# Performance work log

Hardware: AMD Instinct MI355X
Metric: run time of the kernel (lower is better)

The kernel has to match this reference:

```python
import jax, jax.numpy as jnp
import numpy as np

IN_FEATURES = 4096
OUT_FEATURES = 4096
BLOCK_SIZE = 4096
NUM_BLOCKS = 4096
CODEBOOK_SIZE = 256
TOTAL_WEIGHTS = OUT_FEATURES * IN_FEATURES


def setup_inputs() -> dict:
    key = jax.random.key(0)
    k_x, k_cb, k_b, k_idx = jax.random.split(key, 4)
    x = jax.random.normal(k_x, (4, 2048, IN_FEATURES), dtype=jnp.float32)
    codebook = jax.random.normal(k_cb, (NUM_BLOCKS, CODEBOOK_SIZE), dtype=jnp.float32)
    bias = jax.random.normal(k_b, (OUT_FEATURES,), dtype=jnp.float32)
    indices = jax.random.randint(k_idx, (NUM_BLOCKS, BLOCK_SIZE), 0, CODEBOOK_SIZE, dtype=jnp.int64)
    return {"x": x, "codebook": codebook, "bias": bias, "indices": indices}


def reference(x, codebook, bias, indices):
    # weight = codebook[block_idx, indices] : per-block gather of codebook entries
    # codebook: [num_blocks, codebook_size], indices: [num_blocks, block_size]
    w_blocks = jnp.take_along_axis(codebook, indices, axis=1)  # [num_blocks, block_size]
    weight = w_blocks.reshape(-1)[:TOTAL_WEIGHTS].reshape(OUT_FEATURES, IN_FEATURES)
    # F.linear: x @ weight.T + bias
    return jnp.einsum("bsi,oi->bso", x, weight) + bias
```

## Files before the change

### kernel.cpp

```cpp
#include <hip/hip_runtime.h>

typedef __bf16 bf16x8 __attribute__((ext_vector_type(8)));
typedef float f32x4 __attribute__((ext_vector_type(4)));
typedef unsigned short u16x8 __attribute__((ext_vector_type(8)));
typedef int i32x4 __attribute__((ext_vector_type(4)));

#define M_TOT 8192
#define K_TOT 4096
#define N_TOT 4096
#define BM 256
#define BN 256
#define BK 64
#define NT (K_TOT / BK)

__device__ __forceinline__ unsigned short f2bf(float f) {
  union { float f; unsigned int u; } v; v.f = f;
  unsigned int u = v.u;
  return (unsigned short)((u + 0x7FFFu + ((u >> 16) & 1u)) >> 16);
}

__global__ __launch_bounds__(256) void deq_w(const float* __restrict__ cb,
                                             const int* __restrict__ idx,
                                             unsigned short* __restrict__ Wb) {
  size_t base = ((size_t)blockIdx.x * 256 + threadIdx.x) * 8;
  const float* crow = cb + ((base >> 12) << 8);
  i32x4 i0 = *(const i32x4*)(idx + base);
  i32x4 i1 = *(const i32x4*)(idx + base + 4);
  u16x8 o;
#pragma unroll
  for (int j = 0; j < 4; ++j) { o[j] = f2bf(crow[i0[j]]); o[4 + j] = f2bf(crow[i1[j]]); }
  *(u16x8*)(Wb + base) = o;
}

__global__ __launch_bounds__(256) void conv_x(const float* __restrict__ X,
                                              unsigned short* __restrict__ Xc) {
  size_t base = ((size_t)blockIdx.x * 256 + threadIdx.x) * 8;
  f32x4 a = *(const f32x4*)(X + base);
  f32x4 b = *(const f32x4*)(X + base + 4);
  u16x8 o;
#pragma unroll
  for (int j = 0; j < 4; ++j) { o[j] = f2bf(a[j]); o[4 + j] = f2bf(b[j]); }
  *(u16x8*)(Xc + base) = o;
}

#define GLDS16(g, l)                                                      \
  __builtin_amdgcn_global_load_lds(                                       \
      (__attribute__((address_space(1))) void*)(g),                       \
      (__attribute__((address_space(3))) void*)(l), 16, 0, 0)

__global__ __launch_bounds__(512, 2) void gemm8(const unsigned short* __restrict__ A,
                                                const unsigned short* __restrict__ B,
                                                const float* __restrict__ bias,
                                                float* __restrict__ C) {
  __shared__ __attribute__((aligned(128))) char lds[131072];

  const int tid = threadIdx.x;
  const int lane = tid & 63;
  const int wm = (tid >> 6) >> 2;
  const int wn = (tid >> 6) & 3;
  const int lr = lane & 15;

  const int bid = blockIdx.x;
  const int swz = (bid & 7) * 64 + (bid >> 3);
  const int bm = swz >> 4;
  const int bn = swz & 15;

  const unsigned short* Ap = A + (size_t)bm * BM * K_TOT;
  const unsigned short* Bp = B + (size_t)bn * BN * K_TOT;

  const int srow = tid >> 3;
  const int sgcol = (((tid & 7) * 16) ^ ((srow & 7) << 4)) >> 1;
  const int wavebase = (tid & 448) << 4;

  const int cs0 = (((lane >> 4) << 4)) ^ ((lr & 7) << 4);
  const int cs1 = (64 + ((lane >> 4) << 4)) ^ ((lr & 7) << 4);
  const int rowA0 = (wm * 128 + lr) * 128;
  const int rowB0 = 32768 + (wn * 64 + lr) * 128;

#define RD(off) (*(const bf16x8*)(lds + (off)))
#define STAGE(GB, TK, RB, LOFF)                                               \
  { _Pragma("unroll")                                                         \
    for (int ii = 0; ii < 2; ++ii) {                                          \
      GLDS16((GB) + (size_t)((RB) + ii * 64 + srow) * K_TOT + (TK) + sgcol,   \
             lds + (LOFF) + ii * 8192 + wavebase);                            \
    } }
#define BARRIER()                       \
  {                                     \
    asm volatile("" ::: "memory");      \
    __builtin_amdgcn_s_barrier();       \
    asm volatile("" ::: "memory");      \
  }

#define MFMA_Q(MH, AV, BV)                                                    \
  { __builtin_amdgcn_s_setprio(1);                                            \
    _Pragma("unroll")                                                         \
    for (int r = 0; r < 4; ++r) {                                             \
      _Pragma("unroll")                                                       \
      for (int nf = 0; nf < 4; ++nf)                                          \
        acc[(MH) * 4 + r][nf] = __builtin_amdgcn_mfma_f32_16x16x32_bf16(      \
            AV[r], BV[nf], acc[(MH) * 4 + r][nf], 0, 0, 0);                   \
    }                                                                         \
    __builtin_amdgcn_s_setprio(0); }

#define TILE(T, BO, STG_A, STG_B, VMF, DO_BAR)                                    \
  {                                                                               \
    bf16x8 Aa[4], Ab[4], Ac[4], Ad[4], Bx[4], By[4];                              \
    _Pragma("unroll") for (int r = 0; r < 4; ++r)                                 \
        Aa[r] = RD((BO) + rowA0 + r * 2048 + cs0);                                \
    _Pragma("unroll") for (int n = 0; n < 4; ++n)                                 \
        Bx[n] = RD((BO) + rowB0 + n * 2048 + cs0);                                \
    if (STG_A) STAGE(Ap, ((T) + 1) * BK, 0, ((BO) ^ 65536) + 0);                  \
    _Pragma("unroll") for (int r = 0; r < 4; ++r)                                 \
        Ab[r] = RD((BO) + rowA0 + (4 + r) * 2048 + cs0);                          \
    if (STG_A) STAGE(Ap, ((T) + 1) * BK, 128, ((BO) ^ 65536) + 16384);            \
    MFMA_Q(0, Aa, Bx);                                                            \
    _Pragma("unroll") for (int r = 0; r < 4; ++r)                                 \
        Ac[r] = RD((BO) + rowA0 + r * 2048 + cs1);                                \
    _Pragma("unroll") for (int n = 0; n < 4; ++n)                                 \
        By[n] = RD((BO) + rowB0 + n * 2048 + cs1);                                \
    MFMA_Q(1, Ab, Bx);                                                            \
    asm volatile("s_waitcnt lgkmcnt(0)" ::: "memory");                            \
    BARRIER();                                                                    \
    if (STG_B) STAGE(Bp, ((T) + 2) * BK, 0, (BO) + 32768);                        \
    if (STG_B) STAGE(Bp, ((T) + 2) * BK, 128, (BO) + 49152);                      \
    _Pragma("unroll") for (int r = 0; r < 4; ++r)                                 \
        Ad[r] = RD((BO) + rowA0 + (4 + r) * 2048 + cs1);                          \
    MFMA_Q(0, Ac, By);                                                            \
    MFMA_Q(1, Ad, By);                                                            \
    asm volatile("s_waitcnt vmcnt(" VMF ")" ::: "memory");                        \
    if (DO_BAR) BARRIER();                                                        \
  }

  f32x4 acc[8][4] = {};

  STAGE(Bp, 0, 0, 32768);
  STAGE(Bp, 0, 128, 49152);
  STAGE(Ap, 0, 0, 0);
  STAGE(Ap, 0, 128, 16384);
  STAGE(Bp, BK, 0, 65536 + 32768);
  STAGE(Bp, BK, 128, 65536 + 49152);
  asm volatile("s_waitcnt vmcnt(4)" ::: "memory");
  BARRIER();

  for (int t = 0; t < NT - 2; t += 2) {
    TILE(t,     0,     1, 1, "4", 1);
    TILE(t + 1, 65536, 1, 1, "4", 1);
  }
  TILE(NT - 2, 0,     1, 0, "0", 1);
  TILE(NT - 1, 65536, 0, 0, "0", 0);

  const int lg4 = (lane >> 4) << 2;
#pragma unroll
  for (int nf = 0; nf < 4; ++nf) {
    const int col = bn * BN + wn * 64 + nf * 16 + lr;
    const float bv = bias[col];
#pragma unroll
    for (int mf = 0; mf < 8; ++mf) {
      const int row0 = bm * BM + wm * 128 + mf * 16 + lg4;
      float* cp = C + (size_t)row0 * N_TOT + col;
#pragma unroll
      for (int j = 0; j < 4; ++j) cp[(size_t)j * N_TOT] = acc[mf][nf][j] + bv;
    }
  }
#undef RD
#undef STAGE
#undef BARRIER
#undef MFMA_Q
#undef TILE
}

extern "C" void kernel_launch(void* const* d_in, const int* in_sizes, int n_in,
                              void* d_out, int out_size, void* d_ws, size_t ws_size,
                              hipStream_t stream) {
  const float* x    = (const float*)d_in[0];
  const float* cb   = (const float*)d_in[1];
  const float* bias = (const float*)d_in[2];
  const int*   idx  = (const int*)d_in[3];

  float* out = (float*)d_out;

  unsigned short* Wb = (unsigned short*)d_ws;
  unsigned short* Xc = (unsigned short*)((char*)d_ws + (size_t)N_TOT * K_TOT * 2);

  deq_w<<<(N_TOT * (size_t)K_TOT) / (8 * 256), 256, 0, stream>>>(cb, idx, Wb);
  conv_x<<<((size_t)M_TOT * K_TOT) / (8 * 256), 256, 0, stream>>>(x, Xc);
  gemm8<<<512, 512, 0, stream>>>(Xc, Wb, bias, out);
}
```

Baseline: 274.1 us.

## Reorder GEMM tile into quadrant MFMA phases with scheduled LDS interleaving

Restructures each K-tile so every wave loads both K halves of its A and B fragments at once. It then issues MFMAs in four output quadrants, using sched_group_barrier to interleave the next quadrant's LDS reads with the current MFMAs. The B-stage global-to-LDS copies are split across the later quadrants, and the final tile now always ends with a barrier. The goal is to hide LDS read latency behind matrix work and smooth out the instruction mix. The cost is more explicit lgkmcnt waits, and the scheduling hints may not be honoured as intended.

```diff
diff --git a/kernel.cpp b/kernel.cpp
--- a/kernel.cpp
+++ b/kernel.cpp
@@ -90,45 +90,84 @@
     __builtin_amdgcn_s_barrier();       \
     asm volatile("" ::: "memory");      \
   }
-
-#define MFMA_Q(MH, AV, BV)                                                    \
-  { __builtin_amdgcn_s_setprio(1);                                            \
-    _Pragma("unroll")                                                         \
-    for (int r = 0; r < 4; ++r) {                                             \
-      _Pragma("unroll")                                                       \
-      for (int nf = 0; nf < 4; ++nf)                                          \
-        acc[(MH) * 4 + r][nf] = __builtin_amdgcn_mfma_f32_16x16x32_bf16(      \
-            AV[r], BV[nf], acc[(MH) * 4 + r][nf], 0, 0, 0);                   \
-    }                                                                         \
-    __builtin_amdgcn_s_setprio(0); }
-
-#define TILE(T, BO, STG_A, STG_B, VMF, DO_BAR)                                    \
+#define LGKM0() asm volatile("s_waitcnt lgkmcnt(0)" ::: "memory")
+#define SGB(mask, n) __builtin_amdgcn_sched_group_barrier((mask), (n), 0)
+
+#define QMF(MH, NH, AV, BV, MF)                                                          \
+  {                                                                                      \
+    acc[(MH)*4+(MF)][(NH)*2+0] = __builtin_amdgcn_mfma_f32_16x16x32_bf16(                \
+        AV[(MF)*2+0], BV[0], acc[(MH)*4+(MF)][(NH)*2+0], 0, 0, 0);                       \
+    acc[(MH)*4+(MF)][(NH)*2+0] = __builtin_amdgcn_mfma_f32_16x16x32_bf16(                \
+        AV[(MF)*2+1], BV[1], acc[(MH)*4+(MF)][(NH)*2+0], 0, 0, 0);                       \
+    acc[(MH)*4+(MF)][(NH)*2+1] = __builtin_amdgcn_mfma_f32_16x16x32_bf16(                \
+        AV[(MF)*2+0], BV[2], acc[(MH)*4+(MF)][(NH)*2+1], 0, 0, 0);                       \
+    acc[(MH)*4+(MF)][(NH)*2+1] = __builtin_amdgcn_mfma_f32_16x16x32_bf16(                \
+        AV[(MF)*2+1], BV[3], acc[(MH)*4+(MF)][(NH)*2+1], 0, 0, 0);                       \
+  }
+
+#define TILE(T, BO, STG_A, STG_B, VMF)                                            \
   {                                                                               \
-    bf16x8 Aa[4], Ab[4], Ac[4], Ad[4], Bx[4], By[4];                              \
-    _Pragma("unroll") for (int r = 0; r < 4; ++r)                                 \
-        Aa[r] = RD((BO) + rowA0 + r * 2048 + cs0);                                \
-    _Pragma("unroll") for (int n = 0; n < 4; ++n)                                 \
-        Bx[n] = RD((BO) + rowB0 + n * 2048 + cs0);                                \
+    bf16x8 Am[8], Am2[8], Bn[4], Bn2[4];                                          \
+     \
+    _Pragma("unroll") for (int r = 0; r < 4; ++r) {                               \
+      Am[r*2+0] = RD((BO) + rowA0 + r * 2048 + cs0);                              \
+      Am[r*2+1] = RD((BO) + rowA0 + r * 2048 + cs1);                              \
+    }                                                                             \
+    _Pragma("unroll") for (int n = 0; n < 2; ++n) {                               \
+      Bn[n*2+0] = RD((BO) + rowB0 + n * 2048 + cs0);                              \
+      Bn[n*2+1] = RD((BO) + rowB0 + n * 2048 + cs1);                              \
+    }                                                                             \
     if (STG_A) STAGE(Ap, ((T) + 1) * BK, 0, ((BO) ^ 65536) + 0);                  \
-    _Pragma("unroll") for (int r = 0; r < 4; ++r)                                 \
-        Ab[r] = RD((BO) + rowA0 + (4 + r) * 2048 + cs0);                          \
+    LGKM0();                                                                      \
+    __builtin_amdgcn_s_setprio(1);                                                \
+    QMF(0, 0, Am, Bn, 0);                                                         \
+    SGB(0x8, 4);                                                                  \
+    _Pragma("unroll") for (int n = 0; n < 2; ++n) {                               \
+      Bn2[n*2+0] = RD((BO) + rowB0 + 4096 + n * 2048 + cs0);                      \
+      Bn2[n*2+1] = RD((BO) + rowB0 + 4096 + n * 2048 + cs1);                      \
+    }                                                                             \
+    SGB(0x100, 4);                                                                \
+    QMF(0, 0, Am, Bn, 1);                                                         \
+    QMF(0, 0, Am, Bn, 2);                                                         \
+    QMF(0, 0, Am, Bn, 3);                                                         \
+    SGB(0x8, 12);                                                                 \
+    __builtin_amdgcn_s_setprio(0);                                                \
+     \
     if (STG_A) STAGE(Ap, ((T) + 1) * BK, 128, ((BO) ^ 65536) + 16384);            \
-    MFMA_Q(0, Aa, Bx);                                                            \
-    _Pragma("unroll") for (int r = 0; r < 4; ++r)                                 \
-        Ac[r] = RD((BO) + rowA0 + r * 2048 + cs1);                                \
-    _Pragma("unroll") for (int n = 0; n < 4; ++n)                                 \
-        By[n] = RD((BO) + rowB0 + n * 2048 + cs1);                                \
-    MFMA_Q(1, Ab, Bx);                                                            \
-    asm volatile("s_waitcnt lgkmcnt(0)" ::: "memory");                            \
+    LGKM0();                                                                      \
+    __builtin_amdgcn_s_setprio(1);                                                \
+    QMF(0, 1, Am, Bn2, 0);                                                        \
+    SGB(0x8, 4);                                                                  \
+    _Pragma("unroll") for (int r = 0; r < 4; ++r) {                               \
+      Am2[r*2+0] = RD((BO) + rowA0 + 8192 + r * 2048 + cs0);                      \
+      Am2[r*2+1] = RD((BO) + rowA0 + 8192 + r * 2048 + cs1);                      \
+    }                                                                             \
+    SGB(0x100, 8);                                                                \
+    QMF(0, 1, Am, Bn2, 1);                                                        \
+    QMF(0, 1, Am, Bn2, 2);                                                        \
+    QMF(0, 1, Am, Bn2, 3);                                                        \
+    SGB(0x8, 12);                                                                 \
+    __builtin_amdgcn_s_setprio(0);                                                \
+    BARRIER();           \
+     \
+    if (STG_B) STAGE(Bp, ((T) + 2) * BK, 0, (BO) + 32768);                        \
+    LGKM0();                                                                      \
+    __builtin_amdgcn_s_setprio(1);                                                \
+    QMF(1, 0, Am2, Bn, 0);                                                        \
+    QMF(1, 0, Am2, Bn, 1);                                                        \
+    QMF(1, 0, Am2, Bn, 2);                                                        \
+    QMF(1, 0, Am2, Bn, 3);                                                        \
+    __builtin_amdgcn_s_setprio(0);                                                \
+     \
+    if (STG_B) STAGE(Bp, ((T) + 2) * BK, 128, (BO) + 49152);                      \
+    __builtin_amdgcn_s_setprio(1);                                                \
+    QMF(1, 1, Am2, Bn2, 0);                                                       \
+    QMF(1, 1, Am2, Bn2, 1);                                                       \
+    QMF(1, 1, Am2, Bn2, 2);                                                       \
+    QMF(1, 1, Am2, Bn2, 3);                                                       \
+    __builtin_amdgcn_s_setprio(0);                                                \
+    asm volatile("s_waitcnt vmcnt(" VMF ")" ::: "memory");                        \
     BARRIER();                                                                    \
-    if (STG_B) STAGE(Bp, ((T) + 2) * BK, 0, (BO) + 32768);                        \
-    if (STG_B) STAGE(Bp, ((T) + 2) * BK, 128, (BO) + 49152);                      \
-    _Pragma("unroll") for (int r = 0; r < 4; ++r)                                 \
-        Ad[r] = RD((BO) + rowA0 + (4 + r) * 2048 + cs1);                          \
-    MFMA_Q(0, Ac, By);                                                            \
-    MFMA_Q(1, Ad, By);                                                            \
-    asm volatile("s_waitcnt vmcnt(" VMF ")" ::: "memory");                        \
-    if (DO_BAR) BARRIER();                                                        \
   }
 
   f32x4 acc[8][4] = {};
@@ -143,11 +182,11 @@
   BARRIER();
 
   for (int t = 0; t < NT - 2; t += 2) {
-    TILE(t,     0,     1, 1, "4", 1);
-    TILE(t + 1, 65536, 1, 1, "4", 1);
-  }
-  TILE(NT - 2, 0,     1, 0, "0", 1);
-  TILE(NT - 1, 65536, 0, 0, "0", 0);
+    TILE(t,     0,     1, 1, "4");
+    TILE(t + 1, 65536, 1, 1, "4");
+  }
+  TILE(NT - 2, 0,     1, 0, "0");
+  TILE(NT - 1, 65536, 0, 0, "0");
 
   const int lg4 = (lane >> 4) << 2;
 #pragma unroll
@@ -165,7 +204,9 @@
 #undef RD
 #undef STAGE
 #undef BARRIER
-#undef MFMA_Q
+#undef LGKM0
+#undef SGB
+#undef QMF
 #undef TILE
 }
 
```

Result: slower. 284.1 us (+3.6%).

## Load A operand directly from global into registers, halve LDS to B only

Applied to the files above, without the earlier changes.

The GEMM stops staging the activation (A) tile through LDS. Each wave now reads its own A fragments straight from global memory into registers, prefetching the next k-slice while MFMAs run. LDS holds only a double-buffered B tile, which halves LDS use to 64 KB and trims the number of barriers per tile. The cost is that the four waves sharing the same A rows each fetch them separately, using narrow, partly uncoalesced global loads. This adds L2 traffic, raises register pressure, and exposes global-load latency directly to the MFMA loop.

```diff
diff --git a/kernel.cpp b/kernel.cpp
--- a/kernel.cpp
+++ b/kernel.cpp
@@ -52,30 +52,31 @@
                                                 const unsigned short* __restrict__ B,
                                                 const float* __restrict__ bias,
                                                 float* __restrict__ C) {
-  __shared__ __attribute__((aligned(128))) char lds[131072];
+  __shared__ __attribute__((aligned(128))) char lds[65536];
 
   const int tid = threadIdx.x;
   const int lane = tid & 63;
   const int wm = (tid >> 6) >> 2;
   const int wn = (tid >> 6) & 3;
   const int lr = lane & 15;
+  const int kg = lane >> 4;
 
   const int bid = blockIdx.x;
   const int swz = (bid & 7) * 64 + (bid >> 3);
   const int bm = swz >> 4;
   const int bn = swz & 15;
 
-  const unsigned short* Ap = A + (size_t)bm * BM * K_TOT;
+  const unsigned short* Arow =
+      A + ((size_t)(bm * BM + wm * 128 + lr)) * K_TOT + kg * 8;
   const unsigned short* Bp = B + (size_t)bn * BN * K_TOT;
 
   const int srow = tid >> 3;
   const int sgcol = (((tid & 7) * 16) ^ ((srow & 7) << 4)) >> 1;
   const int wavebase = (tid & 448) << 4;
 
-  const int cs0 = (((lane >> 4) << 4)) ^ ((lr & 7) << 4);
-  const int cs1 = (64 + ((lane >> 4) << 4)) ^ ((lr & 7) << 4);
-  const int rowA0 = (wm * 128 + lr) * 128;
-  const int rowB0 = 32768 + (wn * 64 + lr) * 128;
+  const int cs0 = (kg << 4) ^ ((lr & 7) << 4);
+  const int cs1 = (64 + (kg << 4)) ^ ((lr & 7) << 4);
+  const int rowB0 = (wn * 64 + lr) * 128;
 
 #define RD(off) (*(const bf16x8*)(lds + (off)))
 #define STAGE(GB, TK, RB, LOFF)                                               \
@@ -84,6 +85,7 @@
       GLDS16((GB) + (size_t)((RB) + ii * 64 + srow) * K_TOT + (TK) + sgcol,   \
              lds + (LOFF) + ii * 8192 + wavebase);                            \
     } }
+#define CBAR() asm volatile("" ::: "memory")
 #define BARRIER()                       \
   {                                     \
     asm volatile("" ::: "memory");      \
@@ -91,65 +93,60 @@
     asm volatile("" ::: "memory");      \
   }
 
-#define MFMA_Q(MH, AV, BV)                                                    \
+#define MFMA_KH(KH)                                                           \
   { __builtin_amdgcn_s_setprio(1);                                            \
-    _Pragma("unroll")                                                         \
-    for (int r = 0; r < 4; ++r) {                                             \
-      _Pragma("unroll")                                                       \
-      for (int nf = 0; nf < 4; ++nf)                                          \
-        acc[(MH) * 4 + r][nf] = __builtin_amdgcn_mfma_f32_16x16x32_bf16(      \
-            AV[r], BV[nf], acc[(MH) * 4 + r][nf], 0, 0, 0);                   \
+    _Pragma("unroll") for (int mf = 0; mf < 8; ++mf) {                        \
+      _Pragma("unroll") for (int nf = 0; nf < 4; ++nf)                        \
+        acc[mf][nf] = __builtin_amdgcn_mfma_f32_16x16x32_bf16(                \
+            Av[mf], Bv[nf * 2 + (KH)], acc[mf][nf], 0, 0, 0);                 \
     }                                                                         \
     __builtin_amdgcn_s_setprio(0); }
 
-#define TILE(T, BO, STG_A, STG_B, VMF, DO_BAR)                                    \
-  {                                                                               \
-    bf16x8 Aa[4], Ab[4], Ac[4], Ad[4], Bx[4], By[4];                              \
-    _Pragma("unroll") for (int r = 0; r < 4; ++r)                                 \
-        Aa[r] = RD((BO) + rowA0 + r * 2048 + cs0);                                \
-    _Pragma("unroll") for (int n = 0; n < 4; ++n)                                 \
-        Bx[n] = RD((BO) + rowB0 + n * 2048 + cs0);                                \
-    if (STG_A) STAGE(Ap, ((T) + 1) * BK, 0, ((BO) ^ 65536) + 0);                  \
-    _Pragma("unroll") for (int r = 0; r < 4; ++r)                                 \
-        Ab[r] = RD((BO) + rowA0 + (4 + r) * 2048 + cs0);                          \
-    if (STG_A) STAGE(Ap, ((T) + 1) * BK, 128, ((BO) ^ 65536) + 16384);            \
-    MFMA_Q(0, Aa, Bx);                                                            \
-    _Pragma("unroll") for (int r = 0; r < 4; ++r)                                 \
-        Ac[r] = RD((BO) + rowA0 + r * 2048 + cs1);                                \
-    _Pragma("unroll") for (int n = 0; n < 4; ++n)                                 \
-        By[n] = RD((BO) + rowB0 + n * 2048 + cs1);                                \
-    MFMA_Q(1, Ab, Bx);                                                            \
-    asm volatile("s_waitcnt lgkmcnt(0)" ::: "memory");                            \
-    BARRIER();                                                                    \
-    if (STG_B) STAGE(Bp, ((T) + 2) * BK, 0, (BO) + 32768);                        \
-    if (STG_B) STAGE(Bp, ((T) + 2) * BK, 128, (BO) + 49152);                      \
-    _Pragma("unroll") for (int r = 0; r < 4; ++r)                                 \
-        Ad[r] = RD((BO) + rowA0 + (4 + r) * 2048 + cs1);                          \
-    MFMA_Q(0, Ac, By);                                                            \
-    MFMA_Q(1, Ad, By);                                                            \
-    asm volatile("s_waitcnt vmcnt(" VMF ")" ::: "memory");                        \
-    if (DO_BAR) BARRIER();                                                        \
+#define ALOAD(KOFF)                                                           \
+  { _Pragma("unroll") for (int mf = 0; mf < 8; ++mf)                          \
+      Av[mf] = *(const bf16x8*)(Arow + (size_t)mf * 16 * K_TOT + (KOFF)); }
+
+#define TILE(T, BO, STG, PREF)                                                \
+  {                                                                           \
+        \
+    _Pragma("unroll") for (int nf = 0; nf < 4; ++nf) {                        \
+      Bv[nf * 2 + 0] = RD((BO) + rowB0 + nf * 2048 + cs0);                    \
+      Bv[nf * 2 + 1] = RD((BO) + rowB0 + nf * 2048 + cs1);                    \
+    }                                                                         \
+    MFMA_KH(0);                     \
+    ALOAD((T) * BK + 32);            \
+    CBAR();                                                                   \
+    if (STG) {                                                                \
+      STAGE(Bp, ((T) + 1) * BK, 0, ((BO) ^ 32768));                           \
+      STAGE(Bp, ((T) + 1) * BK, 128, ((BO) ^ 32768) + 16384);                 \
+    }                                                                         \
+    CBAR();                                                                   \
+    MFMA_KH(1);                                                               \
+    if (PREF) ALOAD(((T) + 1) * BK);                    \
+    if (STG) {                                                                \
+      asm volatile("s_waitcnt vmcnt(8)" ::: "memory");                        \
+      BARRIER();                                                              \
+    }                                                                         \
   }
 
   f32x4 acc[8][4] = {};
+  bf16x8 Av[8], Bv[8];
 
-  STAGE(Bp, 0, 0, 32768);
-  STAGE(Bp, 0, 128, 49152);
-  STAGE(Ap, 0, 0, 0);
-  STAGE(Ap, 0, 128, 16384);
-  STAGE(Bp, BK, 0, 65536 + 32768);
-  STAGE(Bp, BK, 128, 65536 + 49152);
-  asm volatile("s_waitcnt vmcnt(4)" ::: "memory");
+  STAGE(Bp, 0, 0, 0);
+  STAGE(Bp, 0, 128, 16384);
+  CBAR();
+  ALOAD(0);
+  asm volatile("s_waitcnt vmcnt(8)" ::: "memory");
   BARRIER();
 
   for (int t = 0; t < NT - 2; t += 2) {
-    TILE(t,     0,     1, 1, "4", 1);
-    TILE(t + 1, 65536, 1, 1, "4", 1);
+    TILE(t,     0,     1, 1);
+    TILE(t + 1, 32768, 1, 1);
   }
-  TILE(NT - 2, 0,     1, 0, "0", 1);
-  TILE(NT - 1, 65536, 0, 0, "0", 0);
+  TILE(NT - 2, 0,     1, 1);
+  TILE(NT - 1, 32768, 0, 0);
 
-  const int lg4 = (lane >> 4) << 2;
+  const int lg4 = kg << 2;
 #pragma unroll
   for (int nf = 0; nf < 4; ++nf) {
     const int col = bn * BN + wn * 64 + nf * 16 + lr;
@@ -164,8 +161,10 @@
   }
 #undef RD
 #undef STAGE
+#undef CBAR
 #undef BARRIER
-#undef MFMA_Q
+#undef MFMA_KH
+#undef ALOAD
 #undef TILE
 }
 
```

Measured after the change: 571.3 us. 2.08x slower.

## Fuse prep kernels and simplify GEMM to plain double-buffered pipeline

Applied to the files above, without the earlier changes.

Merges the weight dequant and activation bf16 conversion into one launch, saving a kernel launch and its tail. Replaces the finely interleaved GEMM main loop, which staged A and B at different offsets with two barriers per tile and partial vmcnt waits, with a simple scheme. Each tile now issues all loads for the next tile up front, reads every LDS fragment, runs all MFMAs, then waits on vmcnt(0) and one barrier. This cuts barriers and simplifies scheduling, but loses the fine-grained overlap of LDS reads with MFMAs. It also holds more fragment registers at once, which may pressure occupancy at 2 blocks per CU.

```diff
diff --git a/kernel.cpp b/kernel.cpp
--- a/kernel.cpp
+++ b/kernel.cpp
@@ -19,28 +19,30 @@
   return (unsigned short)((u + 0x7FFFu + ((u >> 16) & 1u)) >> 16);
 }
 
-__global__ __launch_bounds__(256) void deq_w(const float* __restrict__ cb,
-                                             const int* __restrict__ idx,
-                                             unsigned short* __restrict__ Wb) {
-  size_t base = ((size_t)blockIdx.x * 256 + threadIdx.x) * 8;
-  const float* crow = cb + ((base >> 12) << 8);
-  i32x4 i0 = *(const i32x4*)(idx + base);
-  i32x4 i1 = *(const i32x4*)(idx + base + 4);
-  u16x8 o;
+__global__ __launch_bounds__(256) void prep(const float* __restrict__ cb,
+                                            const int* __restrict__ idx,
+                                            const float* __restrict__ X,
+                                            unsigned short* __restrict__ Wb,
+                                            unsigned short* __restrict__ Xc) {
+  const int b = blockIdx.x;
+  if (b < 8192) {
+    size_t base = ((size_t)b * 256 + threadIdx.x) * 8;
+    const float* crow = cb + ((base >> 12) << 8);
+    i32x4 i0 = *(const i32x4*)(idx + base);
+    i32x4 i1 = *(const i32x4*)(idx + base + 4);
+    u16x8 o;
 #pragma unroll
-  for (int j = 0; j < 4; ++j) { o[j] = f2bf(crow[i0[j]]); o[4 + j] = f2bf(crow[i1[j]]); }
-  *(u16x8*)(Wb + base) = o;
-}
-
-__global__ __launch_bounds__(256) void conv_x(const float* __restrict__ X,
-                                              unsigned short* __restrict__ Xc) {
-  size_t base = ((size_t)blockIdx.x * 256 + threadIdx.x) * 8;
-  f32x4 a = *(const f32x4*)(X + base);
-  f32x4 b = *(const f32x4*)(X + base + 4);
-  u16x8 o;
+    for (int j = 0; j < 4; ++j) { o[j] = f2bf(crow[i0[j]]); o[4 + j] = f2bf(crow[i1[j]]); }
+    *(u16x8*)(Wb + base) = o;
+  } else {
+    size_t base = ((size_t)(b - 8192) * 256 + threadIdx.x) * 8;
+    f32x4 a = *(const f32x4*)(X + base);
+    f32x4 c = *(const f32x4*)(X + base + 4);
+    u16x8 o;
 #pragma unroll
-  for (int j = 0; j < 4; ++j) { o[j] = f2bf(a[j]); o[4 + j] = f2bf(b[j]); }
-  *(u16x8*)(Xc + base) = o;
+    for (int j = 0; j < 4; ++j) { o[j] = f2bf(a[j]); o[4 + j] = f2bf(c[j]); }
+    *(u16x8*)(Xc + base) = o;
+  }
 }
 
 #define GLDS16(g, l)                                                      \
@@ -91,63 +93,55 @@
     asm volatile("" ::: "memory");      \
   }
 
-#define MFMA_Q(MH, AV, BV)                                                    \
+#define MFMA_HALF(AV, BV)                                                     \
   { __builtin_amdgcn_s_setprio(1);                                            \
-    _Pragma("unroll")                                                         \
-    for (int r = 0; r < 4; ++r) {                                             \
-      _Pragma("unroll")                                                       \
-      for (int nf = 0; nf < 4; ++nf)                                          \
-        acc[(MH) * 4 + r][nf] = __builtin_amdgcn_mfma_f32_16x16x32_bf16(      \
-            AV[r], BV[nf], acc[(MH) * 4 + r][nf], 0, 0, 0);                   \
+    _Pragma("unroll") for (int mf = 0; mf < 8; ++mf) {                        \
+      _Pragma("unroll") for (int nf = 0; nf < 4; ++nf)                        \
+        acc[mf][nf] = __builtin_amdgcn_mfma_f32_16x16x32_bf16(                \
+            AV[mf], BV[nf], acc[mf][nf], 0, 0, 0);                            \
     }                                                                         \
     __builtin_amdgcn_s_setprio(0); }
 
-#define TILE(T, BO, STG_A, STG_B, VMF, DO_BAR)                                    \
-  {                                                                               \
-    bf16x8 Aa[4], Ab[4], Ac[4], Ad[4], Bx[4], By[4];                              \
-    _Pragma("unroll") for (int r = 0; r < 4; ++r)                                 \
-        Aa[r] = RD((BO) + rowA0 + r * 2048 + cs0);                                \
-    _Pragma("unroll") for (int n = 0; n < 4; ++n)                                 \
-        Bx[n] = RD((BO) + rowB0 + n * 2048 + cs0);                                \
-    if (STG_A) STAGE(Ap, ((T) + 1) * BK, 0, ((BO) ^ 65536) + 0);                  \
-    _Pragma("unroll") for (int r = 0; r < 4; ++r)                                 \
-        Ab[r] = RD((BO) + rowA0 + (4 + r) * 2048 + cs0);                          \
-    if (STG_A) STAGE(Ap, ((T) + 1) * BK, 128, ((BO) ^ 65536) + 16384);            \
-    MFMA_Q(0, Aa, Bx);                                                            \
-    _Pragma("unroll") for (int r = 0; r < 4; ++r)                                 \
-        Ac[r] = RD((BO) + rowA0 + r * 2048 + cs1);                                \
-    _Pragma("unroll") for (int n = 0; n < 4; ++n)                                 \
-        By[n] = RD((BO) + rowB0 + n * 2048 + cs1);                                \
-    MFMA_Q(1, Ab, Bx);                                                            \
-    asm volatile("s_waitcnt lgkmcnt(0)" ::: "memory");                            \
-    BARRIER();                                                                    \
-    if (STG_B) STAGE(Bp, ((T) + 2) * BK, 0, (BO) + 32768);                        \
-    if (STG_B) STAGE(Bp, ((T) + 2) * BK, 128, (BO) + 49152);                      \
-    _Pragma("unroll") for (int r = 0; r < 4; ++r)                                 \
-        Ad[r] = RD((BO) + rowA0 + (4 + r) * 2048 + cs1);                          \
-    MFMA_Q(0, Ac, By);                                                            \
-    MFMA_Q(1, Ad, By);                                                            \
-    asm volatile("s_waitcnt vmcnt(" VMF ")" ::: "memory");                        \
-    if (DO_BAR) BARRIER();                                                        \
+#define TILE(T, BO, STG)                                                      \
+  {                                                                           \
+    if (STG) {                                                                \
+      STAGE(Ap, ((T) + 1) * BK, 0,   ((BO) ^ 65536) + 0);                     \
+      STAGE(Ap, ((T) + 1) * BK, 128, ((BO) ^ 65536) + 16384);                 \
+      STAGE(Bp, ((T) + 1) * BK, 0,   ((BO) ^ 65536) + 32768);                 \
+      STAGE(Bp, ((T) + 1) * BK, 128, ((BO) ^ 65536) + 49152);                 \
+    }                                                                         \
+    bf16x8 Af[8], As[8], Bf[4], Bs[4];                                        \
+    _Pragma("unroll") for (int mf = 0; mf < 8; ++mf)                          \
+        Af[mf] = RD((BO) + rowA0 + mf * 2048 + cs0);                          \
+    _Pragma("unroll") for (int nf = 0; nf < 4; ++nf)                          \
+        Bf[nf] = RD((BO) + rowB0 + nf * 2048 + cs0);                          \
+    _Pragma("unroll") for (int mf = 0; mf < 8; ++mf)                          \
+        As[mf] = RD((BO) + rowA0 + mf * 2048 + cs1);                          \
+    _Pragma("unroll") for (int nf = 0; nf < 4; ++nf)                          \
+        Bs[nf] = RD((BO) + rowB0 + nf * 2048 + cs1);                          \
+    MFMA_HALF(Af, Bf);                                                        \
+    MFMA_HALF(As, Bs);                                                        \
+    if (STG) {                                                                \
+      asm volatile("s_waitcnt vmcnt(0)" ::: "memory");                        \
+      BARRIER();                                                              \
+    }                                                                         \
   }
 
   f32x4 acc[8][4] = {};
 
+  STAGE(Ap, 0, 0, 0);
+  STAGE(Ap, 0, 128, 16384);
   STAGE(Bp, 0, 0, 32768);
   STAGE(Bp, 0, 128, 49152);
-  STAGE(Ap, 0, 0, 0);
-  STAGE(Ap, 0, 128, 16384);
-  STAGE(Bp, BK, 0, 65536 + 32768);
-  STAGE(Bp, BK, 128, 65536 + 49152);
-  asm volatile("s_waitcnt vmcnt(4)" ::: "memory");
+  asm volatile("s_waitcnt vmcnt(0)" ::: "memory");
   BARRIER();
 
   for (int t = 0; t < NT - 2; t += 2) {
-    TILE(t,     0,     1, 1, "4", 1);
-    TILE(t + 1, 65536, 1, 1, "4", 1);
+    TILE(t,     0,     1);
+    TILE(t + 1, 65536, 1);
   }
-  TILE(NT - 2, 0,     1, 0, "0", 1);
-  TILE(NT - 1, 65536, 0, 0, "0", 0);
+  TILE(NT - 2, 0,     1);
+  TILE(NT - 1, 65536, 0);
 
   const int lg4 = (lane >> 4) << 2;
 #pragma unroll
@@ -165,7 +159,7 @@
 #undef RD
 #undef STAGE
 #undef BARRIER
-#undef MFMA_Q
+#undef MFMA_HALF
 #undef TILE
 }
 
@@ -182,7 +176,6 @@
   unsigned short* Wb = (unsigned short*)d_ws;
   unsigned short* Xc = (unsigned short*)((char*)d_ws + (size_t)N_TOT * K_TOT * 2);
 
-  deq_w<<<(N_TOT * (size_t)K_TOT) / (8 * 256), 256, 0, stream>>>(cb, idx, Wb);
-  conv_x<<<((size_t)M_TOT * K_TOT) / (8 * 256), 256, 0, stream>>>(x, Xc);
+  prep<<<24576, 256, 0, stream>>>(cb, idx, x, Wb, Xc);
   gemm8<<<512, 512, 0, stream>>>(Xc, Wb, bias, out);
 }
```

After: 282.5 us. +3.0%, slower.
